# Kernel tuning notes

Hardware: AMD Instinct MI355X
Metric: run time of the kernel (lower is better)

The kernel has to match this reference:

```python
import jax, jax.numpy as jnp
import numpy as np

C = 16; HP = 16; WP = 16; D = 32; KITER = 4; P = 8; N = P * P; B = 16; HID = 64


def conv2d(x, w, b):
    # x: (B, Cin, H, W), w: (Cout, Cin, kh, kw), 'same' padding for 3x3
    y = jax.lax.conv_general_dilated(x, w, (1, 1), [(1, 1), (1, 1)],
                                     dimension_numbers=('NCHW', 'OIHW', 'NCHW'))
    return y + b[None, :, None, None]


def setup_inputs() -> dict:
    key = jax.random.key(0)
    ks = jax.random.split(key, 20)
    n = lambda k, shape, s=0.1: jax.random.normal(k, shape, jnp.float32) * s
    # 4-neighbor directed grid edges over P x P nodes
    edges = []
    for p in range(P):
        for q in range(P):
            i = p * P + q
            for dp, dq in ((0, 1), (1, 0), (0, -1), (-1, 0)):
                pp, qq = p + dp, q + dq
                if 0 <= pp < P and 0 <= qq < P:
                    edges.append((i, pp * P + qq))
    edge_index = jnp.asarray(np.asarray(edges, np.int32))  # (E, 2) with (i=dst, j=src)
    return {
        'seed': n(ks[0], (B, C, P * HP, P * WP), 1.0),
        'edge_index': edge_index,
        'wq': n(ks[1], (C, D)), 'bq': jnp.zeros((D,), jnp.float32),
        'wk': n(ks[2], (C, D)), 'bk': jnp.zeros((D,), jnp.float32),
        'wm': n(ks[3], (C, C, 3, 3)), 'bm': jnp.zeros((C,), jnp.float32),
        'a_w1': n(ks[4], (2 * D, HID)), 'a_b1': jnp.zeros((HID,), jnp.float32),
        'a_w2': n(ks[5], (HID, HID)), 'a_b2': jnp.zeros((HID,), jnp.float32),
        'a_wo': n(ks[6], (HID, 1)), 'a_bo': jnp.zeros((1,), jnp.float32),
        'g_w': n(ks[7], (C, 1, 3, 3)), 'g_b': jnp.zeros((C,), jnp.float32),
        'gru_wg': n(ks[8], (2 * C, 2 * C, 3, 3)), 'gru_bg': jnp.zeros((2 * C,), jnp.float32),
        'gru_wc': n(ks[9], (C, 2 * C, 3, 3)), 'gru_bc': jnp.zeros((C,), jnp.float32),
    }


def reference(seed, edge_index, wq, bq, wk, bk, wm, bm,
              a_w1, a_b1, a_w2, a_b2, a_wo, a_bo,
              g_w, g_b, gru_wg, gru_bg, gru_wc, gru_bc):
    Bb, Cc, PH, PW = seed.shape
    Pp = PH // HP
    Nn = Pp * Pp
    # patchify: (B,C,PH,PW) -> (B,N,C,H,W), node order is row-major (p,q)
    X = seed.reshape(Bb, Cc, Pp, HP, Pp, WP).transpose(0, 2, 4, 1, 3, 5).reshape(Bb, Nn, Cc, HP, WP)
    ei = edge_index[:, 0]  # dst node i
    ej = edge_index[:, 1]  # src node j
    # GateConv on a spatially-constant map e: conv(e*ones) = e * conv(ones) (+bias).
    ones_map = jnp.ones((1, 1, HP, WP), seed.dtype)
    T = jax.lax.conv_general_dilated(ones_map, g_w, (1, 1), [(1, 1), (1, 1)],
                                     dimension_numbers=('NCHW', 'OIHW', 'NCHW'))  # (1,C,H,W)
    for _ in range(KITER):
        xm = X.mean((-2, -1))  # (B,N,C); mean commutes with the 1x1 convs f_Q/f_K
        q_vec = xm @ wq + bq   # (B,N,d)
        k_vec = xm @ wk + bk
        M = conv2d(X.reshape(Bb * Nn, Cc, HP, WP), wm, bm).reshape(Bb, Nn, Cc, HP, WP)
        # per-edge attention scores via ConcatMLP
        h0 = jnp.concatenate([q_vec[:, ei], k_vec[:, ej]], axis=-1)  # (B,E,2d)
        h1 = jax.nn.relu(h0 @ a_w1 + a_b1)
        h2 = jax.nn.relu(h1 @ a_w2 + a_b2)
        e = (h2 @ a_wo + a_bo)[..., 0]  # (B,E)
        # gate map and gated messages
        G = jax.nn.sigmoid(e[:, :, None, None, None] * T[None] + g_b[None, None, :, None, None])  # (B,E,C,H,W)
        msg = G * M[:, ej]  # gather src patches, gate
        agg = jax.ops.segment_sum(jnp.moveaxis(msg, 1, 0), ei, num_segments=Nn)  # (N,B,C,H,W)
        M_agg = jnp.moveaxis(agg, 0, 1).reshape(Bb * Nn, Cc, HP, WP)
        # ConvGRU cell update
        h = X.reshape(Bb * Nn, Cc, HP, WP)
        zr = jax.nn.sigmoid(conv2d(jnp.concatenate([M_agg, h], axis=1), gru_wg, gru_bg))
        z, r = zr[:, :Cc], zr[:, Cc:]
        cand = jnp.tanh(conv2d(jnp.concatenate([M_agg, r * h], axis=1), gru_wc, gru_bc))
        X = ((1.0 - z) * h + z * cand).reshape(Bb, Nn, Cc, HP, WP)
    # unpatchify
    out = X.reshape(Bb, Pp, Pp, Cc, HP, WP).transpose(0, 3, 1, 4, 2, 5).reshape(Bb, Cc, PH, PW)
    return out
```

## Files before the change

kernel.cpp:

```cpp
#include <hip/hip_runtime.h>
#include <hip/hip_bf16.h>

#define Bt 16
#define Ct 16
#define Nt 64
#define KITERt 4

#define WF_TOTAL 25681
#define SWZ_TOTAL 16384
#define SETUP_IDX (WF_TOTAL + 4096 + Nt + SWZ_TOTAL)
#define SAH_STRIDE 40

typedef __attribute__((ext_vector_type(8))) short bf16x8;
typedef __attribute__((ext_vector_type(4))) float f32x4;

__device__ inline float bf2f(__hip_bfloat16 v) { return __bfloat162float(v); }
__device__ inline short f2bs(float f) {
    __hip_bfloat16 h = __float2bfloat16(f);
    short s; __builtin_memcpy(&s, &h, 2); return s;
}
__device__ inline float bs2f(short s) {
    __hip_bfloat16 h; __builtin_memcpy(&h, &s, 2);
    return __bfloat162float(h);
}
__device__ inline float loadf(const void* p, int i, int isf32) {
    return isf32 ? ((const float*)p)[i]
                 : __bfloat162float(((const __hip_bfloat16*)p)[i]);
}
__device__ inline float sigm(float x) {
    return __builtin_amdgcn_rcpf(1.f + __expf(-x));
}
__device__ inline float tanh_fast(float x) {
    float e = __expf(2.f * x);
    return 1.f - 2.f * __builtin_amdgcn_rcpf(e + 1.f);
}

__device__ inline int detect_f32(const void* seed) {
    const __hip_bfloat16* p = (const __hip_bfloat16*)seed;
    float mx = 0.f;
#pragma unroll 8
    for (int k = 0; k < 256; ++k) {
        float v = fabsf(__bfloat162float(p[k]));
        if (!(v <= 1e30f)) v = 1e30f;
        mx = fmaxf(mx, v);
    }
    return mx > 1e10f ? 1 : 0;
}

__global__ __launch_bounds__(256) void setup_kernel(
    const void* __restrict__ seed,
    const void* __restrict__ wq, const void* __restrict__ bq,
    const void* __restrict__ wk, const void* __restrict__ bk,
    const void* __restrict__ wm, const void* __restrict__ bm,
    const void* __restrict__ w1, const void* __restrict__ b1,
    const void* __restrict__ w2, const void* __restrict__ b2,
    const void* __restrict__ wo, const void* __restrict__ bo,
    const void* __restrict__ gw, const void* __restrict__ gb,
    const void* __restrict__ wg, const void* __restrict__ bg,
    const void* __restrict__ wc, const void* __restrict__ bc,
    const int* __restrict__ edge, int E,
    float* __restrict__ Wf, float* __restrict__ Tswz,
    int* __restrict__ counts, int* __restrict__ lists,
    __hip_bfloat16* __restrict__ swz,
    short* __restrict__ Xb, float* __restrict__ qv0, float* __restrict__ kv0,
    int* __restrict__ flag)
{
    __shared__ float xred[64];
    int bn = blockIdx.x, t = threadIdx.x;
    int lane = t & 63, wv = t >> 6;
    int isf32 = detect_f32(seed);
    if (bn == 0 && t == 0) *flag = isf32;

    int idx = bn * 256 + t;
    if (idx < WF_TOTAL) {
        int i = idx;
        const void* base;
        if (i < 512) base = wq;
        else if ((i -= 512) < 32) base = bq;
        else if ((i -= 32) < 512) base = wk;
        else if ((i -= 512) < 32) base = bk;
        else if ((i -= 32) < 2304) base = wm;
        else if ((i -= 2304) < 16) base = bm;
        else if ((i -= 16) < 4096) base = w1;
        else if ((i -= 4096) < 64) base = b1;
        else if ((i -= 64) < 4096) base = w2;
        else if ((i -= 4096) < 64) base = b2;
        else if ((i -= 64) < 64) base = wo;
        else if ((i -= 64) < 1) base = bo;
        else if ((i -= 1) < 16) base = gb;
        else if ((i -= 16) < 9216) base = wg;
        else if ((i -= 9216) < 32) base = bg;
        else if ((i -= 32) < 4608) base = wc;
        else { i -= 4608; base = bc; }
        Wf[idx] = loadf(base, i, isf32);
    } else if (idx < WF_TOTAL + 4096) {
        int j = idx - WF_TOTAL;
        int tt = j >> 4, rr = j & 15;
        int wv2 = tt >> 6, ln = tt & 63, qd = ln >> 4, nn = ln & 15;
        int mt = rr >> 2, r2 = rr & 3;
        int pix = (wv2 * 4 + mt) * 16 + qd * 4 + r2;
        int y = pix >> 4, x = pix & 15;
        float s = 0.f;
        for (int ky = 0; ky < 3; ++ky)
            for (int kx = 0; kx < 3; ++kx) {
                int yy = y + ky - 1, xx = x + kx - 1;
                if (yy >= 0 && yy < 16 && xx >= 0 && xx < 16)
                    s += loadf(gw, nn * 9 + ky * 3 + kx, isf32);
            }
        Tswz[j] = s;
    } else if (idx < WF_TOTAL + 4096 + Nt) {
        int i = idx - WF_TOTAL - 4096;
        int deg = 0;
        for (int e = 0; e < E; ++e)
            if (edge[2 * e] == i) { if (deg < 8) lists[i * 8 + deg] = e; ++deg; }
        counts[i] = deg < 8 ? deg : 8;
    } else if (idx < SETUP_IDX) {
        int j = idx - (WF_TOTAL + 4096 + Nt);
        float val;
        if (j < 9216) {
            int sn = j >> 9, rem = j & 511;
            int ln = rem >> 3, jj = rem & 7;
            int s = sn >> 1, nt = sn & 1;
            int ci = (ln >> 4) * 8 + jj;
            int co = nt * 16 + (ln & 15);
            val = loadf(wg, co * 288 + ci * 9 + s, isf32);
        } else if (j < 9216 + 4608) {
            int j1 = j - 9216;
            int s = j1 >> 9, rem = j1 & 511;
            int ln = rem >> 3, jj = rem & 7;
            int ci = (ln >> 4) * 8 + jj;
            int co = ln & 15;
            val = loadf(wc, co * 288 + ci * 9 + s, isf32);
        } else {
            int j2 = j - 13824;
            int sp = j2 >> 9, rem = j2 & 511;
            int ln = rem >> 3, jj = rem & 7;
            int k = (ln >> 4) * 8 + jj;
            int s = sp * 2 + (k >> 4);
            int ci = k & 15;
            int co = ln & 15;
            val = (s <= 8) ? loadf(wm, co * 144 + ci * 9 + s, isf32) : 0.f;
        }
        swz[j] = __float2bfloat16(val);
    }

    {
        int b = bn >> 6, n = bn & 63;
        int pq = n >> 3, qq = n & 7;
        int y = t >> 4, x = t & 15;
        float v[16];
#pragma unroll
        for (int c = 0; c < 16; ++c)
            v[c] = loadf(seed, ((b * 16 + c) * 128 + pq * 16 + y) * 128 + qq * 16 + x, isf32);
        bf16x8 o0, o1;
#pragma unroll
        for (int c = 0; c < 8; ++c) { o0[c] = f2bs(v[c]); o1[c] = f2bs(v[8 + c]); }
        short* xo = Xb + bn * 4096;
        *(bf16x8*)(xo + t * 16) = o0;
        *(bf16x8*)(xo + t * 16 + 8) = o1;
#pragma unroll
        for (int c = 0; c < 16; ++c) {
            float s = v[c];
#pragma unroll
            for (int off = 1; off < 64; off <<= 1) s += __shfl_xor(s, off, 64);
            if (lane == c) xred[wv * 16 + c] = s;
        }
        __syncthreads();
        if (t < 64) {
            int d = t & 31;
            float a = (t < 32) ? loadf(bq, d, isf32) : loadf(bk, d, isf32);
#pragma unroll
            for (int c = 0; c < 16; ++c) {
                float xm = (xred[c] + xred[16 + c] + xred[32 + c] + xred[48 + c]) * (1.f / 256.f);
                a += xm * ((t < 32) ? loadf(wq, c * 32 + d, isf32)
                                    : loadf(wk, c * 32 + d, isf32));
            }
            if (t < 32) qv0[bn * 32 + d] = a; else kv0[bn * 32 + d] = a;
        }
    }
}

__global__ void pack_kernel(const short* __restrict__ Xb, void* __restrict__ out,
                            const int* __restrict__ flagp)
{
    int isf32 = *flagp;
    int idx = blockIdx.x * 256 + threadIdx.x;
    int xx = idx & 127;
    int rest = idx >> 7;
    int yy = rest & 127; rest >>= 7;
    int c = rest & 15; int b = rest >> 4;
    int n = (yy >> 4) * 8 + (xx >> 4);
    float v = bs2f(Xb[((b * 64 + n) * 256 + (yy & 15) * 16 + (xx & 15)) * 16 + c]);
    if (isf32) ((float*)out)[idx] = v;
    else ((__hip_bfloat16*)out)[idx] = __float2bfloat16(v);
}

__global__ __launch_bounds__(256) void iter_kernel(
    const __hip_bfloat16* __restrict__ Xin, __hip_bfloat16* __restrict__ Xout,
    const float* __restrict__ qin, const float* __restrict__ kin,
    float* __restrict__ qout, float* __restrict__ kout,
    const float* __restrict__ Tswz,
    const short* __restrict__ WmS,
    const short* __restrict__ WgS,
    const short* __restrict__ WcS,
    const float* __restrict__ Wf,
    const int* __restrict__ edge, const int* __restrict__ counts,
    const int* __restrict__ lists, int E)
{
    __shared__ __align__(16) short sAH[324 * SAH_STRIDE];
    __shared__ float evs[8];
    int bn = blockIdx.x, b = bn >> 6, i = bn & 63;
    int t = threadIdx.x, lane = t & 63, wv = t >> 6;
    int quad = lane >> 4, n16 = lane & 15;

    int deg = counts[i];
    if (deg > 4) deg = 4;
    int el[4], ejl[4];
#pragma unroll
    for (int ii = 0; ii < 4; ++ii) {
        int e = (ii < deg) ? lists[i * 8 + ii] : 0;
        el[ii] = e;
        ejl[ii] = (ii < deg) ? edge[2 * e + 1] : 0;
    }
    bf16x8 nbA0, nbA1, nbB0, nbB1;
    if (deg > 0) {
        const short* mp = (const short*)Xin + (b * 64 + ejl[0]) * 4096 + t * 16;
        nbA0 = *(const bf16x8*)(mp);
        nbA1 = *(const bf16x8*)(mp + 8);
    }

    float T_lane[16];
#pragma unroll
    for (int r = 0; r < 16; ++r) T_lane[r] = Tswz[t * 16 + r];
    float gb_l = Wf[11793 + n16];
    float bm_l = Wf[3392 + n16];

    const short* xown = (const short*)Xin + bn * 4096;

    for (int p = t; p < 324; p += 256) {
        int yy = p / 18 - 1, xx = p % 18 - 1;
        short* row = sAH + p * SAH_STRIDE;
        if ((unsigned)yy < 16u && (unsigned)xx < 16u) {
            const short* src = xown + (yy * 16 + xx) * 16;
            *(bf16x8*)(row + 16) = *(const bf16x8*)(src);
            *(bf16x8*)(row + 24) = *(const bf16x8*)(src + 8);
        } else {
            bf16x8 z = {0, 0, 0, 0, 0, 0, 0, 0};
            *(bf16x8*)(row) = z;      *(bf16x8*)(row + 8) = z;
            *(bf16x8*)(row + 16) = z; *(bf16x8*)(row + 24) = z;
        }
    }

    if (wv < deg) {
        int ej = ejl[wv];
        float h0 = (lane < 32) ? qin[bn * 32 + lane]
                               : kin[(b * 64 + ej) * 32 + (lane - 32)];
        const float* W1 = Wf + 3408;
        const float* W2 = Wf + 7568;
        float p0 = 0.f, p1 = 0.f, p2 = 0.f, p3 = 0.f;
#pragma unroll
        for (int j = 0; j < 64; j += 4) {
            p0 += __shfl(h0, j + 0, 64) * W1[(j + 0) * 64 + lane];
            p1 += __shfl(h0, j + 1, 64) * W1[(j + 1) * 64 + lane];
            p2 += __shfl(h0, j + 2, 64) * W1[(j + 2) * 64 + lane];
            p3 += __shfl(h0, j + 3, 64) * W1[(j + 3) * 64 + lane];
        }
        float a1 = fmaxf(Wf[7504 + lane] + ((p0 + p1) + (p2 + p3)), 0.f);
        p0 = p1 = p2 = p3 = 0.f;
#pragma unroll
        for (int j = 0; j < 64; j += 4) {
            p0 += __shfl(a1, j + 0, 64) * W2[(j + 0) * 64 + lane];
            p1 += __shfl(a1, j + 1, 64) * W2[(j + 1) * 64 + lane];
            p2 += __shfl(a1, j + 2, 64) * W2[(j + 2) * 64 + lane];
            p3 += __shfl(a1, j + 3, 64) * W2[(j + 3) * 64 + lane];
        }
        float a2 = fmaxf(Wf[11664 + lane] + ((p0 + p1) + (p2 + p3)), 0.f);
        float pe = a2 * Wf[11728 + lane];
#pragma unroll
        for (int off = 32; off; off >>= 1) pe += __shfl_down(pe, off, 64);
        if (lane == 0) evs[wv] = pe + Wf[11792];
    }
    __syncthreads();

    f32x4 magg[4];
#pragma unroll
    for (int mt = 0; mt < 4; ++mt) magg[mt] = (f32x4){0.f, 0.f, 0.f, 0.f};
    int pp = ((t >> 4) + 1) * 18 + (t & 15) + 1;
    for (int ii = 0; ii < deg; ++ii) {
        *(bf16x8*)(sAH + pp * SAH_STRIDE) = nbA0;
        *(bf16x8*)(sAH + pp * SAH_STRIDE + 8) = nbA1;
        if (ii + 1 < deg) {
            const short* mp = (const short*)Xin + (b * 64 + ejl[ii + 1]) * 4096 + t * 16;
            nbB0 = *(const bf16x8*)(mp);
            nbB1 = *(const bf16x8*)(mp + 8);
        }
        __syncthreads();
        float evv = evs[ii];
        f32x4 acc[4];
#pragma unroll
        for (int mt = 0; mt < 4; ++mt) acc[mt] = (f32x4){bm_l, bm_l, bm_l, bm_l};
#pragma unroll
        for (int sp = 0; sp < 5; ++sp) {
            bf16x8 Bf = *(const bf16x8*)(WmS + sp * 512 + lane * 8);
            int s2 = sp * 2 + (quad >> 1);
            if (s2 > 8) s2 = 8;
            int ky = s2 / 3, kx = s2 - (s2 / 3) * 3;
            int cib = (quad & 1) * 8;
#pragma unroll
            for (int mt = 0; mt < 4; ++mt) {
                int pc = (wv * 4 + mt + ky) * 18 + n16 + kx;
                bf16x8 A = *(const bf16x8*)(sAH + pc * SAH_STRIDE + cib);
                acc[mt] = __builtin_amdgcn_mfma_f32_16x16x32_bf16(A, Bf, acc[mt], 0, 0, 0);
            }
        }
#pragma unroll
        for (int mt = 0; mt < 4; ++mt)
#pragma unroll
            for (int r = 0; r < 4; ++r)
                magg[mt][r] += sigm(evv * T_lane[mt * 4 + r] + gb_l) * acc[mt][r];
        nbA0 = nbB0; nbA1 = nbB1;
        __syncthreads();
    }
#pragma unroll
    for (int mt = 0; mt < 4; ++mt)
#pragma unroll
        for (int r = 0; r < 4; ++r) {
            int p = (wv * 4 + mt + 1) * 18 + quad * 4 + r + 1;
            sAH[p * SAH_STRIDE + n16] = f2bs(magg[mt][r]);
        }
    __syncthreads();

    float bz = Wf[21025 + n16], br = Wf[21025 + 16 + n16];
    f32x4 accZ[4], accR[4];
#pragma unroll
    for (int mt = 0; mt < 4; ++mt) {
        accZ[mt] = (f32x4){bz, bz, bz, bz};
        accR[mt] = (f32x4){br, br, br, br};
    }
#pragma unroll
    for (int s = 0; s < 9; ++s) {
        int ky = s / 3, kx = s - (s / 3) * 3;
        bf16x8 B0 = *(const bf16x8*)(WgS + (s * 2 + 0) * 512 + lane * 8);
        bf16x8 B1 = *(const bf16x8*)(WgS + (s * 2 + 1) * 512 + lane * 8);
#pragma unroll
        for (int mt = 0; mt < 4; ++mt) {
            int pc = (wv * 4 + mt + ky) * 18 + n16 + kx;
            bf16x8 A = *(const bf16x8*)(sAH + pc * SAH_STRIDE + quad * 8);
            accZ[mt] = __builtin_amdgcn_mfma_f32_16x16x32_bf16(A, B0, accZ[mt], 0, 0, 0);
            accR[mt] = __builtin_amdgcn_mfma_f32_16x16x32_bf16(A, B1, accR[mt], 0, 0, 0);
        }
    }
    float zf[16], hf[16], rh[16];
#pragma unroll
    for (int mt = 0; mt < 4; ++mt)
#pragma unroll
        for (int r = 0; r < 4; ++r) {
            int k = mt * 4 + r;
            int ps = (wv * 4 + mt + 1) * 18 + quad * 4 + r + 1;
            hf[k] = bs2f(sAH[ps * SAH_STRIDE + 16 + n16]);
            zf[k] = sigm(accZ[mt][r]);
            rh[k] = sigm(accR[mt][r]) * hf[k];
        }
    __syncthreads();
#pragma unroll
    for (int mt = 0; mt < 4; ++mt)
#pragma unroll
        for (int r = 0; r < 4; ++r) {
            int ps = (wv * 4 + mt + 1) * 18 + quad * 4 + r + 1;
            sAH[ps * SAH_STRIDE + 16 + n16] = f2bs(rh[mt * 4 + r]);
        }
    __syncthreads();

    float bcl = Wf[25665 + n16];
    f32x4 accC[4];
#pragma unroll
    for (int mt = 0; mt < 4; ++mt) accC[mt] = (f32x4){bcl, bcl, bcl, bcl};
#pragma unroll
    for (int s = 0; s < 9; ++s) {
        int ky = s / 3, kx = s - (s / 3) * 3;
        bf16x8 Bc = *(const bf16x8*)(WcS + s * 512 + lane * 8);
#pragma unroll
        for (int mt = 0; mt < 4; ++mt) {
            int pc = (wv * 4 + mt + ky) * 18 + n16 + kx;
            bf16x8 A = *(const bf16x8*)(sAH + pc * SAH_STRIDE + quad * 8);
            accC[mt] = __builtin_amdgcn_mfma_f32_16x16x32_bf16(A, Bc, accC[mt], 0, 0, 0);
        }
    }
    __shared__ float xred[64];
    float ssum = 0.f;
    short* xo = (short*)Xout + bn * 4096;
#pragma unroll
    for (int mt = 0; mt < 4; ++mt)
#pragma unroll
        for (int r = 0; r < 4; ++r) {
            int k = mt * 4 + r;
            float cand = tanh_fast(accC[mt][r]);
            float nx = (1.f - zf[k]) * hf[k] + zf[k] * cand;
            ssum += nx;
            int pix = (wv * 4 + mt) * 16 + quad * 4 + r;
            xo[pix * 16 + n16] = f2bs(nx);
        }
    ssum += __shfl_xor(ssum, 16, 64);
    ssum += __shfl_xor(ssum, 32, 64);
    if (lane < 16) xred[wv * 16 + lane] = ssum;
    __syncthreads();
    if (t < 64) {
        int d = t & 31;
        const float* W = (t < 32) ? Wf : Wf + 544;
        float a = (t < 32) ? Wf[512 + d] : Wf[1056 + d];
#pragma unroll
        for (int c = 0; c < 16; ++c) {
            float xc = (xred[c] + xred[16 + c] + xred[32 + c] + xred[48 + c]) * (1.f / 256.f);
            a += xc * W[c * 32 + d];
        }
        if (t < 32) qout[bn * 32 + d] = a; else kout[bn * 32 + d] = a;
    }
}

extern "C" void kernel_launch(void* const* d_in, const int* in_sizes, int n_in,
                              void* d_out, int out_size, void* d_ws, size_t ws_size,
                              hipStream_t stream)
{
    const void* seed = d_in[0];
    const int* edge = (const int*)d_in[1];
    int E = in_sizes[1] / 2;

    float* ws = (float*)d_ws;
    short* Xb0 = (short*)ws;
    short* Xb1 = (short*)d_out;
    float* qv0 = ws + 2097152;
    float* kv0 = qv0 + 32768;
    float* qv1 = kv0 + 32768;
    float* kv1 = qv1 + 32768;
    float* Tswz = kv1 + 32768;
    float* Wf = Tswz + 4096;
    int* flag = (int*)(Wf + WF_TOTAL);
    int* counts = flag + 16;
    int* lists = counts + 64;
    __hip_bfloat16* swz = (__hip_bfloat16*)(ws + 2260000);

    const short* WgS = (const short*)swz;
    const short* WcS = (const short*)(swz + 9216);
    const short* WmS = (const short*)(swz + 13824);

    setup_kernel<<<Bt * Nt, 256, 0, stream>>>(
        seed,
        d_in[2], d_in[3], d_in[4], d_in[5], d_in[6], d_in[7], d_in[8], d_in[9],
        d_in[10], d_in[11], d_in[12], d_in[13], d_in[14], d_in[15], d_in[16],
        d_in[17], d_in[18], d_in[19],
        edge, E, Wf, Tswz, counts, lists, swz, Xb0, qv0, kv0, flag);

    short* Xs[2] = {Xb0, Xb1};
    float* qs[2] = {qv0, qv1};
    float* ks[2] = {kv0, kv1};
    for (int it = 0; it < KITERt; ++it) {
        int in = it & 1, on = in ^ 1;
        iter_kernel<<<Bt * Nt, 256, 0, stream>>>(
            (const __hip_bfloat16*)Xs[in], (__hip_bfloat16*)Xs[on],
            qs[in], ks[in], qs[on], ks[on],
            Tswz, WmS, WgS, WcS, Wf, edge, counts, lists, E);
    }

    pack_kernel<<<out_size / 256, 256, 0, stream>>>(Xs[KITERt & 1], d_out, flag);
}
```

Before: 276.2 us.

## Fuse unpatchify into last iteration, prefetch neighbours into LDS, simplify setup

Removes the separate pack kernel by writing the final iteration's output directly in NCHW layout from the iteration kernel. Neighbour patches are now loaded up front into registers and staged through a double-buffered LDS area, and the message conv reads that buffer directly with clamped, masked indexing. The halo padding rows are dropped from the GRU staging buffer and replaced by row clamping plus zero masks. Setup now detects the input dtype with one parallel warp reduction instead of a per-thread serial loop, and precomputes source-node IDs rather than edge IDs. Together these cut one launch and some global and LDS traffic, at the cost of more registers (launch bounds 256,4) and a larger LDS footprint.

```diff
diff --git a/kernel.cpp b/kernel.cpp
--- a/kernel.cpp
+++ b/kernel.cpp
@@ -12,6 +12,7 @@
 #define SAH_STRIDE 40
 
 typedef __attribute__((ext_vector_type(8))) short bf16x8;
+typedef __attribute__((ext_vector_type(4))) short s16x4;
 typedef __attribute__((ext_vector_type(4))) float f32x4;
 
 __device__ inline float bf2f(__hip_bfloat16 v) { return __bfloat162float(v); }
@@ -33,18 +34,6 @@
 __device__ inline float tanh_fast(float x) {
     float e = __expf(2.f * x);
     return 1.f - 2.f * __builtin_amdgcn_rcpf(e + 1.f);
-}
-
-__device__ inline int detect_f32(const void* seed) {
-    const __hip_bfloat16* p = (const __hip_bfloat16*)seed;
-    float mx = 0.f;
-#pragma unroll 8
-    for (int k = 0; k < 256; ++k) {
-        float v = fabsf(__bfloat162float(p[k]));
-        if (!(v <= 1e30f)) v = 1e30f;
-        mx = fmaxf(mx, v);
-    }
-    return mx > 1e10f ? 1 : 0;
 }
 
 __global__ __launch_bounds__(256) void setup_kernel(
@@ -60,16 +49,32 @@
     const void* __restrict__ wc, const void* __restrict__ bc,
     const int* __restrict__ edge, int E,
     float* __restrict__ Wf, float* __restrict__ Tswz,
-    int* __restrict__ counts, int* __restrict__ lists,
+    int* __restrict__ counts, int* __restrict__ nbrs,
     __hip_bfloat16* __restrict__ swz,
     short* __restrict__ Xb, float* __restrict__ qv0, float* __restrict__ kv0,
     int* __restrict__ flag)
 {
+    __shared__ float sred[4];
+    __shared__ int sflag;
     __shared__ float xred[64];
     int bn = blockIdx.x, t = threadIdx.x;
     int lane = t & 63, wv = t >> 6;
-    int isf32 = detect_f32(seed);
-    if (bn == 0 && t == 0) *flag = isf32;
+
+    {
+        float v = fabsf(__bfloat162float(((const __hip_bfloat16*)seed)[t]));
+        if (!(v <= 1e30f)) v = 1e30f;
+#pragma unroll
+        for (int off = 1; off < 64; off <<= 1) v = fmaxf(v, __shfl_xor(v, off, 64));
+        if (lane == 0) sred[wv] = v;
+        __syncthreads();
+        if (t == 0) {
+            float m = fmaxf(fmaxf(sred[0], sred[1]), fmaxf(sred[2], sred[3]));
+            sflag = (m > 1e10f) ? 1 : 0;
+            if (bn == 0) *flag = sflag;
+        }
+        __syncthreads();
+    }
+    int isf32 = sflag;
 
     int idx = bn * 256 + t;
     if (idx < WF_TOTAL) {
@@ -112,8 +117,9 @@
         int i = idx - WF_TOTAL - 4096;
         int deg = 0;
         for (int e = 0; e < E; ++e)
-            if (edge[2 * e] == i) { if (deg < 8) lists[i * 8 + deg] = e; ++deg; }
-        counts[i] = deg < 8 ? deg : 8;
+            if (edge[2 * e] == i && deg < 4) { nbrs[i * 4 + deg] = edge[2 * e + 1]; ++deg; }
+        for (int ii = deg; ii < 4; ++ii) nbrs[i * 4 + ii] = 0;
+        counts[i] = deg;
     } else if (idx < SETUP_IDX) {
         int j = idx - (WF_TOTAL + 4096 + Nt);
         float val;
@@ -180,23 +186,8 @@
     }
 }
 
-__global__ void pack_kernel(const short* __restrict__ Xb, void* __restrict__ out,
-                            const int* __restrict__ flagp)
-{
-    int isf32 = *flagp;
-    int idx = blockIdx.x * 256 + threadIdx.x;
-    int xx = idx & 127;
-    int rest = idx >> 7;
-    int yy = rest & 127; rest >>= 7;
-    int c = rest & 15; int b = rest >> 4;
-    int n = (yy >> 4) * 8 + (xx >> 4);
-    float v = bs2f(Xb[((b * 64 + n) * 256 + (yy & 15) * 16 + (xx & 15)) * 16 + c]);
-    if (isf32) ((float*)out)[idx] = v;
-    else ((__hip_bfloat16*)out)[idx] = __float2bfloat16(v);
-}
-
-__global__ __launch_bounds__(256) void iter_kernel(
-    const __hip_bfloat16* __restrict__ Xin, __hip_bfloat16* __restrict__ Xout,
+__global__ __launch_bounds__(256, 4) void iter_kernel(
+    const short* __restrict__ Xin, short* __restrict__ Xout,
     const float* __restrict__ qin, const float* __restrict__ kin,
     float* __restrict__ qout, float* __restrict__ kout,
     const float* __restrict__ Tswz,
@@ -204,29 +195,31 @@
     const short* __restrict__ WgS,
     const short* __restrict__ WcS,
     const float* __restrict__ Wf,
-    const int* __restrict__ edge, const int* __restrict__ counts,
-    const int* __restrict__ lists, int E)
+    const int* __restrict__ counts, const int* __restrict__ nbrs,
+    const int* __restrict__ flagp, void* __restrict__ out, int last)
 {
-    __shared__ __align__(16) short sAH[324 * SAH_STRIDE];
-    __shared__ float evs[8];
+    __shared__ __align__(16) short sAH[288 * SAH_STRIDE];
+    __shared__ __align__(16) short sNB[2][4096];
+    __shared__ float evs[4];
+    __shared__ float xred[64];
     int bn = blockIdx.x, b = bn >> 6, i = bn & 63;
     int t = threadIdx.x, lane = t & 63, wv = t >> 6;
     int quad = lane >> 4, n16 = lane & 15;
 
+    int4 nb4 = *(const int4*)(nbrs + i * 4);
     int deg = counts[i];
-    if (deg > 4) deg = 4;
-    int el[4], ejl[4];
+    int ejl[4] = {nb4.x, nb4.y, nb4.z, nb4.w};
+    const short* xown = Xin + bn * 4096;
+    bf16x8 own0 = *(const bf16x8*)(xown + t * 16);
+    bf16x8 own1 = *(const bf16x8*)(xown + t * 16 + 8);
+    bf16x8 nA[4], nB[4];
 #pragma unroll
     for (int ii = 0; ii < 4; ++ii) {
-        int e = (ii < deg) ? lists[i * 8 + ii] : 0;
-        el[ii] = e;
-        ejl[ii] = (ii < deg) ? edge[2 * e + 1] : 0;
-    }
-    bf16x8 nbA0, nbA1, nbB0, nbB1;
-    if (deg > 0) {
-        const short* mp = (const short*)Xin + (b * 64 + ejl[0]) * 4096 + t * 16;
-        nbA0 = *(const bf16x8*)(mp);
-        nbA1 = *(const bf16x8*)(mp + 8);
+        if (ii < deg) {
+            const short* mp = Xin + (b * 64 + ejl[ii]) * 4096 + t * 16;
+            nA[ii] = *(const bf16x8*)(mp);
+            nB[ii] = *(const bf16x8*)(mp + 8);
+        }
     }
 
     float T_lane[16];
@@ -235,19 +228,21 @@
     float gb_l = Wf[11793 + n16];
     float bm_l = Wf[3392 + n16];
 
-    const short* xown = (const short*)Xin + bn * 4096;
-
-    for (int p = t; p < 324; p += 256) {
-        int yy = p / 18 - 1, xx = p % 18 - 1;
-        short* row = sAH + p * SAH_STRIDE;
-        if ((unsigned)yy < 16u && (unsigned)xx < 16u) {
-            const short* src = xown + (yy * 16 + xx) * 16;
-            *(bf16x8*)(row + 16) = *(const bf16x8*)(src);
-            *(bf16x8*)(row + 24) = *(const bf16x8*)(src + 8);
-        } else {
+    {
+        int y = t >> 4, x = t & 15;
+        short* row = sAH + (y * 18 + x + 1) * SAH_STRIDE;
+        *(bf16x8*)(row + 16) = own0;
+        *(bf16x8*)(row + 24) = own1;
+        if (t < 32) {
+            int yy = t & 15, col = (t >> 4) * 17;
+            short* br = sAH + (yy * 18 + col) * SAH_STRIDE;
             bf16x8 z = {0, 0, 0, 0, 0, 0, 0, 0};
-            *(bf16x8*)(row) = z;      *(bf16x8*)(row + 8) = z;
-            *(bf16x8*)(row + 16) = z; *(bf16x8*)(row + 24) = z;
+            *(bf16x8*)(br) = z;      *(bf16x8*)(br + 8) = z;
+            *(bf16x8*)(br + 16) = z; *(bf16x8*)(br + 24) = z;
+        }
+        if (deg > 0) {
+            *(bf16x8*)(&sNB[0][t * 16]) = nA[0];
+            *(bf16x8*)(&sNB[0][t * 16 + 8]) = nB[0];
         }
     }
 
@@ -285,16 +280,14 @@
     f32x4 magg[4];
 #pragma unroll
     for (int mt = 0; mt < 4; ++mt) magg[mt] = (f32x4){0.f, 0.f, 0.f, 0.f};
-    int pp = ((t >> 4) + 1) * 18 + (t & 15) + 1;
-    for (int ii = 0; ii < deg; ++ii) {
-        *(bf16x8*)(sAH + pp * SAH_STRIDE) = nbA0;
-        *(bf16x8*)(sAH + pp * SAH_STRIDE + 8) = nbA1;
+#pragma unroll
+    for (int ii = 0; ii < 4; ++ii) {
+        if (ii >= deg) break;
+        const short* buf = sNB[ii & 1];
         if (ii + 1 < deg) {
-            const short* mp = (const short*)Xin + (b * 64 + ejl[ii + 1]) * 4096 + t * 16;
-            nbB0 = *(const bf16x8*)(mp);
-            nbB1 = *(const bf16x8*)(mp + 8);
-        }
-        __syncthreads();
+            *(bf16x8*)(&sNB[(ii + 1) & 1][t * 16]) = nA[ii + 1];
+            *(bf16x8*)(&sNB[(ii + 1) & 1][t * 16 + 8]) = nB[ii + 1];
+        }
         float evv = evs[ii];
         f32x4 acc[4];
 #pragma unroll
@@ -304,12 +297,16 @@
             bf16x8 Bf = *(const bf16x8*)(WmS + sp * 512 + lane * 8);
             int s2 = sp * 2 + (quad >> 1);
             if (s2 > 8) s2 = 8;
-            int ky = s2 / 3, kx = s2 - (s2 / 3) * 3;
+            int ky = s2 / 3 - 1, kx = s2 - (s2 / 3) * 3 - 1;
             int cib = (quad & 1) * 8;
 #pragma unroll
             for (int mt = 0; mt < 4; ++mt) {
-                int pc = (wv * 4 + mt + ky) * 18 + n16 + kx;
-                bf16x8 A = *(const bf16x8*)(sAH + pc * SAH_STRIDE + cib);
+                int py = wv * 4 + mt + ky, px = n16 + kx;
+                bool ok = ((unsigned)py < 16u) & ((unsigned)px < 16u);
+                int pyc = py < 0 ? 0 : (py > 15 ? 15 : py);
+                int pxc = px < 0 ? 0 : (px > 15 ? 15 : px);
+                bf16x8 A = *(const bf16x8*)(buf + (pyc * 16 + pxc) * 16 + cib);
+                if (!ok) A = (bf16x8){0, 0, 0, 0, 0, 0, 0, 0};
                 acc[mt] = __builtin_amdgcn_mfma_f32_16x16x32_bf16(A, Bf, acc[mt], 0, 0, 0);
             }
         }
@@ -318,14 +315,13 @@
 #pragma unroll
             for (int r = 0; r < 4; ++r)
                 magg[mt][r] += sigm(evv * T_lane[mt * 4 + r] + gb_l) * acc[mt][r];
-        nbA0 = nbB0; nbA1 = nbB1;
         __syncthreads();
     }
 #pragma unroll
     for (int mt = 0; mt < 4; ++mt)
 #pragma unroll
         for (int r = 0; r < 4; ++r) {
-            int p = (wv * 4 + mt + 1) * 18 + quad * 4 + r + 1;
+            int p = (wv * 4 + mt) * 18 + quad * 4 + r + 1;
             sAH[p * SAH_STRIDE + n16] = f2bs(magg[mt][r]);
         }
     __syncthreads();
@@ -344,8 +340,10 @@
         bf16x8 B1 = *(const bf16x8*)(WgS + (s * 2 + 1) * 512 + lane * 8);
 #pragma unroll
         for (int mt = 0; mt < 4; ++mt) {
-            int pc = (wv * 4 + mt + ky) * 18 + n16 + kx;
-            bf16x8 A = *(const bf16x8*)(sAH + pc * SAH_STRIDE + quad * 8);
+            int py = wv * 4 + mt + ky - 1;
+            int pyc = py < 0 ? 0 : (py > 15 ? 15 : py);
+            bf16x8 A = *(const bf16x8*)(sAH + (pyc * 18 + n16 + kx) * SAH_STRIDE + quad * 8);
+            if ((unsigned)py >= 16u) A = (bf16x8){0, 0, 0, 0, 0, 0, 0, 0};
             accZ[mt] = __builtin_amdgcn_mfma_f32_16x16x32_bf16(A, B0, accZ[mt], 0, 0, 0);
             accR[mt] = __builtin_amdgcn_mfma_f32_16x16x32_bf16(A, B1, accR[mt], 0, 0, 0);
         }
@@ -356,7 +354,7 @@
 #pragma unroll
         for (int r = 0; r < 4; ++r) {
             int k = mt * 4 + r;
-            int ps = (wv * 4 + mt + 1) * 18 + quad * 4 + r + 1;
+            int ps = (wv * 4 + mt) * 18 + quad * 4 + r + 1;
             hf[k] = bs2f(sAH[ps * SAH_STRIDE + 16 + n16]);
             zf[k] = sigm(accZ[mt][r]);
             rh[k] = sigm(accR[mt][r]) * hf[k];
@@ -366,7 +364,7 @@
     for (int mt = 0; mt < 4; ++mt)
 #pragma unroll
         for (int r = 0; r < 4; ++r) {
-            int ps = (wv * 4 + mt + 1) * 18 + quad * 4 + r + 1;
+            int ps = (wv * 4 + mt) * 18 + quad * 4 + r + 1;
             sAH[ps * SAH_STRIDE + 16 + n16] = f2bs(rh[mt * 4 + r]);
         }
     __syncthreads();
@@ -381,39 +379,65 @@
         bf16x8 Bc = *(const bf16x8*)(WcS + s * 512 + lane * 8);
 #pragma unroll
         for (int mt = 0; mt < 4; ++mt) {
-            int pc = (wv * 4 + mt + ky) * 18 + n16 + kx;
-            bf16x8 A = *(const bf16x8*)(sAH + pc * SAH_STRIDE + quad * 8);
+            int py = wv * 4 + mt + ky - 1;
+            int pyc = py < 0 ? 0 : (py > 15 ? 15 : py);
+            bf16x8 A = *(const bf16x8*)(sAH + (pyc * 18 + n16 + kx) * SAH_STRIDE + quad * 8);
+            if ((unsigned)py >= 16u) A = (bf16x8){0, 0, 0, 0, 0, 0, 0, 0};
             accC[mt] = __builtin_amdgcn_mfma_f32_16x16x32_bf16(A, Bc, accC[mt], 0, 0, 0);
         }
     }
-    __shared__ float xred[64];
-    float ssum = 0.f;
-    short* xo = (short*)Xout + bn * 4096;
+    float nxv[16];
 #pragma unroll
     for (int mt = 0; mt < 4; ++mt)
 #pragma unroll
         for (int r = 0; r < 4; ++r) {
             int k = mt * 4 + r;
-            float cand = tanh_fast(accC[mt][r]);
-            float nx = (1.f - zf[k]) * hf[k] + zf[k] * cand;
-            ssum += nx;
-            int pix = (wv * 4 + mt) * 16 + quad * 4 + r;
-            xo[pix * 16 + n16] = f2bs(nx);
-        }
-    ssum += __shfl_xor(ssum, 16, 64);
-    ssum += __shfl_xor(ssum, 32, 64);
-    if (lane < 16) xred[wv * 16 + lane] = ssum;
-    __syncthreads();
-    if (t < 64) {
-        int d = t & 31;
-        const float* W = (t < 32) ? Wf : Wf + 544;
-        float a = (t < 32) ? Wf[512 + d] : Wf[1056 + d];
-#pragma unroll
-        for (int c = 0; c < 16; ++c) {
-            float xc = (xred[c] + xred[16 + c] + xred[32 + c] + xred[48 + c]) * (1.f / 256.f);
-            a += xc * W[c * 32 + d];
-        }
-        if (t < 32) qout[bn * 32 + d] = a; else kout[bn * 32 + d] = a;
+            nxv[k] = (1.f - zf[k]) * hf[k] + zf[k] * tanh_fast(accC[mt][r]);
+        }
+
+    if (!last) {
+        short* xo = Xout + bn * 4096;
+        float ssum = 0.f;
+#pragma unroll
+        for (int mt = 0; mt < 4; ++mt)
+#pragma unroll
+            for (int r = 0; r < 4; ++r) {
+                int k = mt * 4 + r;
+                ssum += nxv[k];
+                int pix = (wv * 4 + mt) * 16 + quad * 4 + r;
+                xo[pix * 16 + n16] = f2bs(nxv[k]);
+            }
+        ssum += __shfl_xor(ssum, 16, 64);
+        ssum += __shfl_xor(ssum, 32, 64);
+        if (lane < 16) xred[wv * 16 + lane] = ssum;
+        __syncthreads();
+        if (t < 64) {
+            int d = t & 31;
+            const float* W = (t < 32) ? Wf : Wf + 544;
+            float a = (t < 32) ? Wf[512 + d] : Wf[1056 + d];
+#pragma unroll
+            for (int c = 0; c < 16; ++c) {
+                float xc = (xred[c] + xred[16 + c] + xred[32 + c] + xred[48 + c]) * (1.f / 256.f);
+                a += xc * W[c * 32 + d];
+            }
+            if (t < 32) qout[bn * 32 + d] = a; else kout[bn * 32 + d] = a;
+        }
+    } else {
+        int isf32 = *flagp;
+        int pq = i >> 3, qq = i & 7;
+#pragma unroll
+        for (int mt = 0; mt < 4; ++mt) {
+            long base = ((long)(b * 16 + n16) * 128 + pq * 16 + wv * 4 + mt) * 128
+                        + qq * 16 + quad * 4;
+            if (isf32) {
+                f32x4 v = {nxv[mt * 4], nxv[mt * 4 + 1], nxv[mt * 4 + 2], nxv[mt * 4 + 3]};
+                *(f32x4*)((float*)out + base) = v;
+            } else {
+                s16x4 v = {f2bs(nxv[mt * 4]), f2bs(nxv[mt * 4 + 1]),
+                           f2bs(nxv[mt * 4 + 2]), f2bs(nxv[mt * 4 + 3])};
+                *(s16x4*)((short*)out + base) = v;
+            }
+        }
     }
 }
 
@@ -427,17 +451,17 @@
 
     float* ws = (float*)d_ws;
     short* Xb0 = (short*)ws;
-    short* Xb1 = (short*)d_out;
-    float* qv0 = ws + 2097152;
+    short* Xb1 = (short*)(ws + 2097152);
+    float* qv0 = ws + 4194304;
     float* kv0 = qv0 + 32768;
     float* qv1 = kv0 + 32768;
     float* kv1 = qv1 + 32768;
     float* Tswz = kv1 + 32768;
     float* Wf = Tswz + 4096;
-    int* flag = (int*)(Wf + WF_TOTAL);
-    int* counts = flag + 16;
-    int* lists = counts + 64;
-    __hip_bfloat16* swz = (__hip_bfloat16*)(ws + 2260000);
+    int* nbrs = (int*)(ws + 4355168);
+    int* counts = nbrs + 256;
+    int* flag = counts + 64;
+    __hip_bfloat16* swz = (__hip_bfloat16*)(ws + 4355600);
 
     const short* WgS = (const short*)swz;
     const short* WcS = (const short*)(swz + 9216);
@@ -448,18 +472,16 @@
         d_in[2], d_in[3], d_in[4], d_in[5], d_in[6], d_in[7], d_in[8], d_in[9],
         d_in[10], d_in[11], d_in[12], d_in[13], d_in[14], d_in[15], d_in[16],
         d_in[17], d_in[18], d_in[19],
-        edge, E, Wf, Tswz, counts, lists, swz, Xb0, qv0, kv0, flag);
+        edge, E, Wf, Tswz, counts, nbrs, swz, Xb0, qv0, kv0, flag);
 
     short* Xs[2] = {Xb0, Xb1};
     float* qs[2] = {qv0, qv1};
     float* ks[2] = {kv0, kv1};
     for (int it = 0; it < KITERt; ++it) {
         int in = it & 1, on = in ^ 1;
+        int last = (it == KITERt - 1);
         iter_kernel<<<Bt * Nt, 256, 0, stream>>>(
-            (const __hip_bfloat16*)Xs[in], (__hip_bfloat16*)Xs[on],
-            qs[in], ks[in], qs[on], ks[on],
-            Tswz, WmS, WgS, WcS, Wf, edge, counts, lists, E);
-    }
-
-    pack_kernel<<<out_size / 256, 256, 0, stream>>>(Xs[KITERt & 1], d_out, flag);
-}
+            Xs[in], Xs[on], qs[in], ks[in], qs[on], ks[on],
+            Tswz, WmS, WgS, WcS, Wf, counts, nbrs, flag, d_out, last);
+    }
+}
```

After: 347.8 us. 25.9% more time.
